# Kernel optimization log

Measured on AMD Instinct MI355X. Metric: run time of the kernel, lower is better.

The kernel has to match this reference:

```python
import jax, jax.numpy as jnp
import numpy as np

B, T, C, NH, RD = 128, 512, 384, 6, 16
HD = C // NH
SEQ_LEN = 512


def setup_inputs() -> dict:
    key = jax.random.key(0)
    kx, kqkv, kout = jax.random.split(key, 3)
    x = jax.random.normal(kx, (B, T, C), dtype=jnp.float32)
    # torch nn.Linear weights are [out_features, in_features]
    Wqkv = jax.random.normal(kqkv, (3 * C, C), dtype=jnp.float32) * 0.02
    Wout = jax.random.normal(kout, (C, C), dtype=jnp.float32) * 0.02
    freqs = 1.0 / (10000.0 ** (jnp.arange(0, RD, 2, dtype=jnp.float32) / RD))  # [RD//2]
    f = jnp.outer(jnp.arange(SEQ_LEN, dtype=jnp.float32), freqs)  # [SEQ_LEN, RD//2]
    cos = jnp.cos(f)[None, None]  # [1,1,SEQ_LEN,RD//2]
    sin = jnp.sin(f)[None, None]
    return {"x": x, "Wqkv": Wqkv, "Wout": Wout, "cos": cos, "sin": sin}


def _rope(t, c, s, rd):
    # t: [B, NH, T, HD]; partial rotary on first rd channels
    r, p = t[..., :rd], t[..., rd:]
    r1, r2 = r[..., : rd // 2], r[..., rd // 2:]
    rot = jnp.concatenate([r1 * c - r2 * s, r2 * c + r1 * s], axis=-1)
    return jnp.concatenate([rot, p], axis=-1)


def reference(x, Wqkv, Wout, cos, sin):
    b, t, c = x.shape
    nh, hd, rd = NH, c // NH, RD
    qkv = jnp.einsum("btc,dc->btd", x, Wqkv).reshape(b, t, 3, nh, hd)
    q, k, v = (jnp.transpose(qkv[:, :, i], (0, 2, 1, 3)) for i in range(3))  # [b,nh,t,hd]
    cc = cos[:, :, :t]
    ss = sin[:, :, :t]
    q = _rope(q, cc, ss, rd)
    k = _rope(k, cc, ss, rd)
    scale = 1.0 / jnp.sqrt(jnp.asarray(hd, dtype=x.dtype))
    scores = jnp.einsum("bhqd,bhkd->bhqk", q, k) * scale
    causal = jnp.tril(jnp.ones((t, t), dtype=bool))
    scores = jnp.where(causal, scores, jnp.finfo(scores.dtype).min)
    att = jax.nn.softmax(scores, axis=-1)
    o = jnp.einsum("bhqk,bhkd->bhqd", att, v)  # [b,nh,t,hd]
    o = jnp.transpose(o, (0, 2, 1, 3)).reshape(b, t, c)
    return jnp.einsum("btc,dc->btd", o, Wout)
```

## Files before the change

### kernel.cpp

```cpp
#include <hip/hip_runtime.h>

#define B_DIM 128
#define T_DIM 512
#define C_DIM 384
#define NH_DIM 6
#define HD_DIM 64
#define QKV_LD 1152

typedef __bf16 bf16x8 __attribute__((ext_vector_type(8)));
typedef __bf16 bf16x4 __attribute__((ext_vector_type(4)));
typedef float f32x4 __attribute__((ext_vector_type(4)));

#define K_SCALE 0.18033688011112042f

__device__ __forceinline__ void gload_lds16(const __bf16* g, __bf16* l) {
  __builtin_amdgcn_global_load_lds(
      (const __attribute__((address_space(1))) void*)g,
      (__attribute__((address_space(3))) void*)l, 16, 0, 0);
}

#define X_F4 6291456
#define WQKV_F4 110592
#define WOUT_F4 36864
__global__ __launch_bounds__(256) void cast_all(const float* __restrict__ x,
                                                const float* __restrict__ wqkv,
                                                const float* __restrict__ wout,
                                                __bf16* __restrict__ xb,
                                                __bf16* __restrict__ wqkvb,
                                                __bf16* __restrict__ woutb) {
  int i = blockIdx.x * blockDim.x + threadIdx.x;
  const float4* src;
  bf16x4* dst;
  if (i < X_F4) {
    src = (const float4*)x + i;
    dst = (bf16x4*)xb + i;
  } else if (i < X_F4 + WQKV_F4) {
    src = (const float4*)wqkv + (i - X_F4);
    dst = (bf16x4*)wqkvb + (i - X_F4);
  } else {
    src = (const float4*)wout + (i - X_F4 - WQKV_F4);
    dst = (bf16x4*)woutb + (i - X_F4 - WQKV_F4);
  }
  float4 v = *src;
  bf16x4 o;
  o[0] = (__bf16)v.x; o[1] = (__bf16)v.y; o[2] = (__bf16)v.z; o[3] = (__bf16)v.w;
  *dst = o;
}

__global__ __launch_bounds__(256) void gemm_bt(const __bf16* __restrict__ A,
                                               const __bf16* __restrict__ Bm,
                                               __bf16* __restrict__ Cb,
                                               float* __restrict__ Cf,
                                               const float* __restrict__ cosp,
                                               const float* __restrict__ sinp,
                                               int M, int N, int K) {
  __shared__ __attribute__((aligned(16))) __bf16 As[128 * 32];
  __shared__ __attribute__((aligned(16))) __bf16 Bs[128 * 32];
  const int nwg = gridDim.x * gridDim.y;
  const int bid = blockIdx.x + gridDim.x * blockIdx.y;
  const int per = nwg >> 3;
  const int swz = (bid & 7) * per + (bid >> 3);
  const int m0 = (swz / gridDim.x) * 128;
  const int n0 = (swz % gridDim.x) * 128;
  const int tid = threadIdx.x;
  const int wave = tid >> 6;
  const int lane = tid & 63;
  const int lr = lane & 15;
  const int quad = lane >> 4;
  const int wm = (wave & 1) * 64;
  const int wn = (wave >> 1) * 64;
  const int ca0 = wave * 2, ca1 = wave * 2 + 1;
  const int srow = lane >> 2;
  const int row0 = ca0 * 16 + srow, row1 = ca1 * 16 + srow;
  const int slot = (lane & 3) ^ ((lane >> 3) & 3);
  const int rs = (quad ^ ((lr >> 1) & 3)) * 8;
  f32x4 acc[4][4] = {};
  for (int k0 = 0; k0 < K; k0 += 32) {
    __syncthreads();
    gload_lds16(&A[(size_t)(m0 + row0) * K + k0 + slot * 8], &As[ca0 * 512]);
    gload_lds16(&A[(size_t)(m0 + row1) * K + k0 + slot * 8], &As[ca1 * 512]);
    gload_lds16(&Bm[(size_t)(n0 + row0) * K + k0 + slot * 8], &Bs[ca0 * 512]);
    gload_lds16(&Bm[(size_t)(n0 + row1) * K + k0 + slot * 8], &Bs[ca1 * 512]);
    __syncthreads();
    bf16x8 af[4], bf[4];
#pragma unroll
    for (int i = 0; i < 4; ++i)
      af[i] = *(bf16x8*)&As[(wm + i * 16 + lr) * 32 + rs];
#pragma unroll
    for (int j = 0; j < 4; ++j)
      bf[j] = *(bf16x8*)&Bs[(wn + j * 16 + lr) * 32 + rs];
#pragma unroll
    for (int i = 0; i < 4; ++i)
#pragma unroll
      for (int j = 0; j < 4; ++j)
        acc[i][j] = __builtin_amdgcn_mfma_f32_16x16x32_bf16(af[i], bf[j], acc[i][j], 0, 0, 0);
  }
  const bool doRope = (cosp != nullptr);
#pragma unroll
  for (int i = 0; i < 4; ++i) {
#pragma unroll
    for (int j = 0; j < 4; ++j) {
      int gm = m0 + wm + i * 16 + quad * 4;
      int gn = n0 + wn + j * 16 + lr;
      if (Cf) {
#pragma unroll
        for (int r = 0; r < 4; ++r) Cf[(size_t)(gm + r) * N + gn] = acc[i][j][r];
      } else {
        const int cbase = n0 + wn + j * 16;
        const bool ropeBlk = doRope && (cbase < 2 * C_DIM) && ((cbase & 63) == 0);
        const float qs = (doRope && cbase < C_DIM) ? K_SCALE : 1.0f;
        if (ropeBlk) {
#pragma unroll
          for (int r = 0; r < 4; ++r) {
            float v = acc[i][j][r];
            float p = __shfl_xor(v, 8, 64);
            int t = (gm + r) & (T_DIM - 1);
            float c = cosp[t * 8 + (lr & 7)];
            float s = sinp[t * 8 + (lr & 7)];
            v = (lr & 8) ? __builtin_fmaf(v, c, p * s)
                         : __builtin_fmaf(v, c, -p * s);
            Cb[(size_t)(gm + r) * N + gn] = (__bf16)(v * qs);
          }
        } else {
#pragma unroll
          for (int r = 0; r < 4; ++r)
            Cb[(size_t)(gm + r) * N + gn] = (__bf16)(acc[i][j][r] * qs);
        }
      }
    }
  }
}

__global__ __launch_bounds__(256) void transpose_v(const __bf16* __restrict__ qkv,
                                                   __bf16* __restrict__ vt) {
  __shared__ __attribute__((aligned(16))) __bf16 Tl[64][72];
  const int tt = blockIdx.x;
  const int h = blockIdx.y;
  const int b = blockIdx.z;
  const int tid = threadIdx.x;
  const __bf16* src = qkv + (size_t)b * T_DIM * QKV_LD + 2 * C_DIM + h * HD_DIM;
#pragma unroll
  for (int i = 0; i < 2; ++i) {
    int c = tid + i * 256;
    int row = c >> 3, cc = (c & 7) * 8;
    *(bf16x8*)&Tl[row][cc] = *(const bf16x8*)&src[(size_t)(tt * 64 + row) * QKV_LD + cc];
  }
  __syncthreads();
  __bf16* dst = vt + (size_t)(b * NH_DIM + h) * HD_DIM * T_DIM + tt * 64;
#pragma unroll
  for (int i = 0; i < 2; ++i) {
    int c = tid + i * 256;
    int drow = c >> 3, tc = (c & 7) * 8;
    bf16x8 v;
#pragma unroll
    for (int j = 0; j < 8; ++j) v[j] = Tl[tc + j][drow];
    *(bf16x8*)&dst[(size_t)drow * T_DIM + tc] = v;
  }
}

__global__ __launch_bounds__(256) void attn_kernel(const __bf16* __restrict__ qkv,
                                                   const __bf16* __restrict__ vt,
                                                   __bf16* __restrict__ o) {
  __shared__ __attribute__((aligned(16))) __bf16 K0s[64 * 64];
  __shared__ __attribute__((aligned(16))) __bf16 K1s[64 * 64];
  __shared__ __attribute__((aligned(16))) __bf16 V0s[64 * 64];
  __shared__ __attribute__((aligned(16))) __bf16 V1s[64 * 64];
  const int bid = blockIdx.x;
  const int swz = (bid & 7) * 384 + (bid >> 3);
  const int pair = swz & 3;
  const int h = (swz >> 2) % NH_DIM;
  const int b = swz / (4 * NH_DIM);
  const int qlo = pair, qhi = 7 - pair;
  const int tid = threadIdx.x;
  const int wave = tid >> 6;
  const int lane = tid & 63;
  const int lr = lane & 15;
  const int quad = lane >> 4;
  const __bf16* qbase = qkv + (size_t)b * T_DIM * QKV_LD + h * HD_DIM;
  const __bf16* kbase = qbase + C_DIM;
  const __bf16* vtb = vt + (size_t)(b * NH_DIM + h) * HD_DIM * T_DIM;
  const int qrow_lo = qlo * 64 + wave * 16;
  const int qrow_hi = qhi * 64 + wave * 16;
  bf16x8 qfl[2], qfh[2];
#pragma unroll
  for (int ks = 0; ks < 2; ++ks) {
    qfl[ks] = *(const bf16x8*)&qbase[(size_t)(qrow_lo + lr) * QKV_LD + ks * 32 + quad * 8];
    qfh[ks] = *(const bf16x8*)&qbase[(size_t)(qrow_hi + lr) * QKV_LD + ks * 32 + quad * 8];
  }
  f32x4 oaL[4] = {}, oaH[4] = {};
  f32x4 lL = {}, lH = {};
  bf16x8 vones;
#pragma unroll
  for (int e = 0; e < 8; ++e) vones[e] = (__bf16)1.0f;
  const int skey = (((lane >> 3) & 3) << 1) | (wave & 1);
  const int gsl = ((lane & 7) ^ skey) * 8;
  const int grA = wave * 8 + (lane >> 3);
  const int grB = grA + 32;
  const int ldsA = wave * 512;
  const int ldsB = (wave + 4) * 512;
  auto stage = [&](int kt, __bf16* KT, __bf16* VT) {
    const __bf16* ks = kbase + (size_t)(kt * 64) * QKV_LD;
    const __bf16* vs = vtb + kt * 64;
    gload_lds16(&ks[(size_t)grA * QKV_LD + gsl], KT + ldsA);
    gload_lds16(&ks[(size_t)grB * QKV_LD + gsl], KT + ldsB);
    gload_lds16(&vs[(size_t)grA * T_DIM + gsl], VT + ldsA);
    gload_lds16(&vs[(size_t)grB * T_DIM + gsl], VT + ldsB);
  };
  const int keyK = ((lr & 3) << 1) | ((lr >> 2) & 1);
  const int keyV = ((lr & 3) << 1) | ((lr >> 3) & 1);
  const int swK0 = (quad ^ keyK) * 8, swK1 = ((4 + quad) ^ keyK) * 8;
  const int swV0 = (quad ^ keyV) * 8, swV1 = ((4 + quad) ^ keyV) * 8;
  const int rkbase = ((lr >> 2) & 3) * 8 + (lr & 3);
  auto body = [&](const __bf16* KT, const __bf16* VT, const bf16x8 (&qf)[2],
                  f32x4 (&oa)[4], f32x4& lacc, int myq, bool diag, int kt) {
    f32x4 sj[4];
#pragma unroll
    for (int j = 0; j < 4; ++j) {
      const int rK = (j >> 1) * 32 + (j & 1) * 4 + rkbase;
      bf16x8 kf0 = *(const bf16x8*)&KT[rK * 64 + swK0];
      bf16x8 kf1 = *(const bf16x8*)&KT[rK * 64 + swK1];
      f32x4 z = {};
      z = __builtin_amdgcn_mfma_f32_16x16x32_bf16(kf0, qf[0], z, 0, 0, 0);
      z = __builtin_amdgcn_mfma_f32_16x16x32_bf16(kf1, qf[1], z, 0, 0, 0);
      sj[j] = z;
    }
    if (diag) {
#pragma unroll
      for (int j = 0; j < 4; ++j)
#pragma unroll
        for (int r = 0; r < 4; ++r) {
          int key = kt * 64 + (j >> 1) * 32 + quad * 8 + (j & 1) * 4 + r;
          if (key > myq) sj[j][r] = -3.0e38f;
        }
    }
    bf16x8 pf0, pf1;
#pragma unroll
    for (int j = 0; j < 4; ++j)
#pragma unroll
      for (int r = 0; r < 4; ++r) {
        float pv = exp2f(sj[j][r]);
        const int jj = (j & 1) * 4 + r;
        if (j < 2) pf0[jj] = (__bf16)pv; else pf1[jj] = (__bf16)pv;
      }
#pragma unroll
    for (int dt = 0; dt < 4; ++dt) {
      bf16x8 vf0 = *(const bf16x8*)&VT[(dt * 16 + lr) * 64 + swV0];
      bf16x8 vf1 = *(const bf16x8*)&VT[(dt * 16 + lr) * 64 + swV1];
      oa[dt] = __builtin_amdgcn_mfma_f32_16x16x32_bf16(pf0, vf0, oa[dt], 0, 0, 0);
      oa[dt] = __builtin_amdgcn_mfma_f32_16x16x32_bf16(pf1, vf1, oa[dt], 0, 0, 0);
    }
    lacc = __builtin_amdgcn_mfma_f32_16x16x32_bf16(pf0, vones, lacc, 0, 0, 0);
    lacc = __builtin_amdgcn_mfma_f32_16x16x32_bf16(pf1, vones, lacc, 0, 0, 0);
  };
  stage(0, K0s, V0s);
  __syncthreads();
  int kt = 0;
  while (true) {
    if (kt < qhi) stage(kt + 1, K1s, V1s);
    if (kt <= qlo) body(K0s, V0s, qfl, oaL, lL, qrow_lo + lr, kt == qlo, kt);
    body(K0s, V0s, qfh, oaH, lH, qrow_hi + lr, kt == qhi, kt);
    __syncthreads();
    ++kt;
    if (kt > qhi) break;
    if (kt < qhi) stage(kt + 1, K0s, V0s);
    if (kt <= qlo) body(K1s, V1s, qfl, oaL, lL, qrow_lo + lr, kt == qlo, kt);
    body(K1s, V1s, qfh, oaH, lH, qrow_hi + lr, kt == qhi, kt);
    __syncthreads();
    ++kt;
    if (kt > qhi) break;
  }
#pragma unroll
  for (int r = 0; r < 4; ++r) {
    float ilL = 1.0f / lL[r];
    float ilH = 1.0f / lH[r];
#pragma unroll
    for (int dt = 0; dt < 4; ++dt) {
      size_t rowL = (size_t)b * T_DIM + qrow_lo + quad * 4 + r;
      size_t rowH = (size_t)b * T_DIM + qrow_hi + quad * 4 + r;
      o[rowL * C_DIM + h * HD_DIM + dt * 16 + lr] = (__bf16)(oaL[dt][r] * ilL);
      o[rowH * C_DIM + h * HD_DIM + dt * 16 + lr] = (__bf16)(oaH[dt][r] * ilH);
    }
  }
}

extern "C" void kernel_launch(void* const* d_in, const int* in_sizes, int n_in,
                              void* d_out, int out_size, void* d_ws, size_t ws_size,
                              hipStream_t stream) {
  const float* x    = (const float*)d_in[0];
  const float* wqkv = (const float*)d_in[1];
  const float* wout = (const float*)d_in[2];
  const float* cosp = (const float*)d_in[3];
  const float* sinp = (const float*)d_in[4];
  float* out = (float*)d_out;

  char* ws = (char*)d_ws;
  __bf16* xb    = (__bf16*)(ws);
  __bf16* wqkvb = (__bf16*)(ws + 50331648);
  __bf16* woutb = (__bf16*)(ws + 51216384);
  __bf16* qkvb  = (__bf16*)(ws + 51511296);
  __bf16* ob    = (__bf16*)(ws + 202506240);
  __bf16* vtb   = xb;

  const int M = B_DIM * T_DIM;

  cast_all<<<25152, 256, 0, stream>>>(x, wqkv, wout, xb, wqkvb, woutb);

  gemm_bt<<<dim3(QKV_LD / 128, M / 128), 256, 0, stream>>>(
      xb, wqkvb, qkvb, (float*)nullptr, cosp, sinp, M, QKV_LD, C_DIM);

  transpose_v<<<dim3(T_DIM / 64, NH_DIM, B_DIM), 256, 0, stream>>>(qkvb, vtb);

  attn_kernel<<<3072, 256, 0, stream>>>(qkvb, vtb, ob);

  gemm_bt<<<dim3(C_DIM / 128, M / 128), 256, 0, stream>>>(
      ob, woutb, (__bf16*)nullptr, out, (const float*)nullptr, (const float*)nullptr,
      M, C_DIM, C_DIM);
}
```

Measured before the change: 401.4 us.

## Fuse V transpose into QKV GEMM epilogue and split Q/K outputs

The QKV GEMM epilogue now writes Q and K into separate contiguous [B*T, C] buffers and, for V column tiles, transposes the accumulator through LDS and writes V directly in the [b,h,d,t] layout. This removes the separate transpose_v kernel launch and its read/write of V, and the attention kernel reads Q/K with a smaller row stride. The GEMM's A/B pointers are also precomputed and incremented per K step. In exchange, the V-tile epilogue adds two LDS passes with extra barriers, and the workspace layout is reorganised.

```diff
diff --git a/kernel.cpp b/kernel.cpp
--- a/kernel.cpp
+++ b/kernel.cpp
@@ -49,7 +49,9 @@
 
 __global__ __launch_bounds__(256) void gemm_bt(const __bf16* __restrict__ A,
                                                const __bf16* __restrict__ Bm,
-                                               __bf16* __restrict__ Cb,
+                                               __bf16* __restrict__ Cbq,
+                                               __bf16* __restrict__ Cbk,
+                                               __bf16* __restrict__ vt,
                                                float* __restrict__ Cf,
                                                const float* __restrict__ cosp,
                                                const float* __restrict__ sinp,
@@ -74,13 +76,18 @@
   const int row0 = ca0 * 16 + srow, row1 = ca1 * 16 + srow;
   const int slot = (lane & 3) ^ ((lane >> 3) & 3);
   const int rs = (quad ^ ((lr >> 1) & 3)) * 8;
+  const __bf16* pA0 = &A[(size_t)(m0 + row0) * K + slot * 8];
+  const __bf16* pA1 = &A[(size_t)(m0 + row1) * K + slot * 8];
+  const __bf16* pB0 = &Bm[(size_t)(n0 + row0) * K + slot * 8];
+  const __bf16* pB1 = &Bm[(size_t)(n0 + row1) * K + slot * 8];
   f32x4 acc[4][4] = {};
   for (int k0 = 0; k0 < K; k0 += 32) {
     __syncthreads();
-    gload_lds16(&A[(size_t)(m0 + row0) * K + k0 + slot * 8], &As[ca0 * 512]);
-    gload_lds16(&A[(size_t)(m0 + row1) * K + k0 + slot * 8], &As[ca1 * 512]);
-    gload_lds16(&Bm[(size_t)(n0 + row0) * K + k0 + slot * 8], &Bs[ca0 * 512]);
-    gload_lds16(&Bm[(size_t)(n0 + row1) * K + k0 + slot * 8], &Bs[ca1 * 512]);
+    gload_lds16(pA0, &As[ca0 * 512]);
+    gload_lds16(pA1, &As[ca1 * 512]);
+    gload_lds16(pB0, &Bs[ca0 * 512]);
+    gload_lds16(pB1, &Bs[ca1 * 512]);
+    pA0 += 32; pA1 += 32; pB0 += 32; pB1 += 32;
     __syncthreads();
     bf16x8 af[4], bf[4];
 #pragma unroll
@@ -95,70 +102,87 @@
       for (int j = 0; j < 4; ++j)
         acc[i][j] = __builtin_amdgcn_mfma_f32_16x16x32_bf16(af[i], bf[j], acc[i][j], 0, 0, 0);
   }
-  const bool doRope = (cosp != nullptr);
+  if (Cf) {
+#pragma unroll
+    for (int i = 0; i < 4; ++i)
+#pragma unroll
+      for (int j = 0; j < 4; ++j) {
+        int gm = m0 + wm + i * 16 + quad * 4;
+        int gn = n0 + wn + j * 16 + lr;
+#pragma unroll
+        for (int r = 0; r < 4; ++r) Cf[(size_t)(gm + r) * N + gn] = acc[i][j][r];
+      }
+    return;
+  }
+  if (n0 >= 2 * C_DIM) {
+    const int tbase = (m0 & (T_DIM - 1)) + wm;
+    const int bb = m0 >> 9;
+    const int dcolbase = n0 - 2 * C_DIM + wn;
+    const int tslotx = (lane & 7) ^ (lane >> 3);
+#pragma unroll
+    for (int pass = 0; pass < 2; ++pass) {
+      __syncthreads();
+      if ((wave >> 1) == pass) {
+        __bf16* T = (wave & 1) ? Bs : As;
+#pragma unroll
+        for (int i = 0; i < 4; ++i)
+#pragma unroll
+          for (int j = 0; j < 4; ++j) {
+            const int d = j * 16 + lr;
+            const int sl = (i * 2 + (quad >> 1)) ^ (d & 7);
+            bf16x4 w;
+#pragma unroll
+            for (int r = 0; r < 4; ++r) w[r] = (__bf16)acc[i][j][r];
+            *(bf16x4*)&T[d * 64 + sl * 8 + (quad & 1) * 4] = w;
+          }
+#pragma unroll
+        for (int it = 0; it < 8; ++it) {
+          const int dl = it * 8 + (lane >> 3);
+          bf16x8 v = *(bf16x8*)&T[dl * 64 + (lane & 7) * 8];
+          const int dfull = dcolbase + dl;
+          const int hh = dfull >> 6, dd = dfull & 63;
+          *(bf16x8*)&vt[((size_t)(bb * NH_DIM + hh) * 64 + dd) * T_DIM + tbase +
+                        tslotx * 8] = v;
+        }
+      }
+    }
+    return;
+  }
+  const bool isQ = (n0 < C_DIM);
+  __bf16* dst = isQ ? Cbq : Cbk;
+  const int colbase = n0 - (isQ ? 0 : C_DIM);
+  const float qs = isQ ? K_SCALE : 1.0f;
 #pragma unroll
   for (int i = 0; i < 4; ++i) {
 #pragma unroll
     for (int j = 0; j < 4; ++j) {
       int gm = m0 + wm + i * 16 + quad * 4;
-      int gn = n0 + wn + j * 16 + lr;
-      if (Cf) {
-#pragma unroll
-        for (int r = 0; r < 4; ++r) Cf[(size_t)(gm + r) * N + gn] = acc[i][j][r];
+      int gn = colbase + wn + j * 16 + lr;
+      const int cbase = colbase + wn + j * 16;
+      const bool ropeBlk = ((cbase & 63) == 0);
+      if (ropeBlk) {
+#pragma unroll
+        for (int r = 0; r < 4; ++r) {
+          float v = acc[i][j][r];
+          float p = __shfl_xor(v, 8, 64);
+          int t = (gm + r) & (T_DIM - 1);
+          float c = cosp[t * 8 + (lr & 7)];
+          float s = sinp[t * 8 + (lr & 7)];
+          v = (lr & 8) ? __builtin_fmaf(v, c, p * s)
+                       : __builtin_fmaf(v, c, -p * s);
+          dst[(size_t)(gm + r) * C_DIM + gn] = (__bf16)(v * qs);
+        }
       } else {
-        const int cbase = n0 + wn + j * 16;
-        const bool ropeBlk = doRope && (cbase < 2 * C_DIM) && ((cbase & 63) == 0);
-        const float qs = (doRope && cbase < C_DIM) ? K_SCALE : 1.0f;
-        if (ropeBlk) {
-#pragma unroll
-          for (int r = 0; r < 4; ++r) {
-            float v = acc[i][j][r];
-            float p = __shfl_xor(v, 8, 64);
-            int t = (gm + r) & (T_DIM - 1);
-            float c = cosp[t * 8 + (lr & 7)];
-            float s = sinp[t * 8 + (lr & 7)];
-            v = (lr & 8) ? __builtin_fmaf(v, c, p * s)
-                         : __builtin_fmaf(v, c, -p * s);
-            Cb[(size_t)(gm + r) * N + gn] = (__bf16)(v * qs);
-          }
-        } else {
-#pragma unroll
-          for (int r = 0; r < 4; ++r)
-            Cb[(size_t)(gm + r) * N + gn] = (__bf16)(acc[i][j][r] * qs);
-        }
+#pragma unroll
+        for (int r = 0; r < 4; ++r)
+          dst[(size_t)(gm + r) * C_DIM + gn] = (__bf16)(acc[i][j][r] * qs);
       }
     }
   }
 }
 
-__global__ __launch_bounds__(256) void transpose_v(const __bf16* __restrict__ qkv,
-                                                   __bf16* __restrict__ vt) {
-  __shared__ __attribute__((aligned(16))) __bf16 Tl[64][72];
-  const int tt = blockIdx.x;
-  const int h = blockIdx.y;
-  const int b = blockIdx.z;
-  const int tid = threadIdx.x;
-  const __bf16* src = qkv + (size_t)b * T_DIM * QKV_LD + 2 * C_DIM + h * HD_DIM;
-#pragma unroll
-  for (int i = 0; i < 2; ++i) {
-    int c = tid + i * 256;
-    int row = c >> 3, cc = (c & 7) * 8;
-    *(bf16x8*)&Tl[row][cc] = *(const bf16x8*)&src[(size_t)(tt * 64 + row) * QKV_LD + cc];
-  }
-  __syncthreads();
-  __bf16* dst = vt + (size_t)(b * NH_DIM + h) * HD_DIM * T_DIM + tt * 64;
-#pragma unroll
-  for (int i = 0; i < 2; ++i) {
-    int c = tid + i * 256;
-    int drow = c >> 3, tc = (c & 7) * 8;
-    bf16x8 v;
-#pragma unroll
-    for (int j = 0; j < 8; ++j) v[j] = Tl[tc + j][drow];
-    *(bf16x8*)&dst[(size_t)drow * T_DIM + tc] = v;
-  }
-}
-
-__global__ __launch_bounds__(256) void attn_kernel(const __bf16* __restrict__ qkv,
+__global__ __launch_bounds__(256) void attn_kernel(const __bf16* __restrict__ qb,
+                                                   const __bf16* __restrict__ kb,
                                                    const __bf16* __restrict__ vt,
                                                    __bf16* __restrict__ o) {
   __shared__ __attribute__((aligned(16))) __bf16 K0s[64 * 64];
@@ -176,16 +200,16 @@
   const int lane = tid & 63;
   const int lr = lane & 15;
   const int quad = lane >> 4;
-  const __bf16* qbase = qkv + (size_t)b * T_DIM * QKV_LD + h * HD_DIM;
-  const __bf16* kbase = qbase + C_DIM;
+  const __bf16* qbase = qb + (size_t)b * T_DIM * C_DIM + h * HD_DIM;
+  const __bf16* kbase = kb + (size_t)b * T_DIM * C_DIM + h * HD_DIM;
   const __bf16* vtb = vt + (size_t)(b * NH_DIM + h) * HD_DIM * T_DIM;
   const int qrow_lo = qlo * 64 + wave * 16;
   const int qrow_hi = qhi * 64 + wave * 16;
   bf16x8 qfl[2], qfh[2];
 #pragma unroll
   for (int ks = 0; ks < 2; ++ks) {
-    qfl[ks] = *(const bf16x8*)&qbase[(size_t)(qrow_lo + lr) * QKV_LD + ks * 32 + quad * 8];
-    qfh[ks] = *(const bf16x8*)&qbase[(size_t)(qrow_hi + lr) * QKV_LD + ks * 32 + quad * 8];
+    qfl[ks] = *(const bf16x8*)&qbase[(size_t)(qrow_lo + lr) * C_DIM + ks * 32 + quad * 8];
+    qfh[ks] = *(const bf16x8*)&qbase[(size_t)(qrow_hi + lr) * C_DIM + ks * 32 + quad * 8];
   }
   f32x4 oaL[4] = {}, oaH[4] = {};
   f32x4 lL = {}, lH = {};
@@ -199,10 +223,10 @@
   const int ldsA = wave * 512;
   const int ldsB = (wave + 4) * 512;
   auto stage = [&](int kt, __bf16* KT, __bf16* VT) {
-    const __bf16* ks = kbase + (size_t)(kt * 64) * QKV_LD;
+    const __bf16* ks = kbase + (size_t)(kt * 64) * C_DIM;
     const __bf16* vs = vtb + kt * 64;
-    gload_lds16(&ks[(size_t)grA * QKV_LD + gsl], KT + ldsA);
-    gload_lds16(&ks[(size_t)grB * QKV_LD + gsl], KT + ldsB);
+    gload_lds16(&ks[(size_t)grA * C_DIM + gsl], KT + ldsA);
+    gload_lds16(&ks[(size_t)grB * C_DIM + gsl], KT + ldsB);
     gload_lds16(&vs[(size_t)grA * T_DIM + gsl], VT + ldsA);
     gload_lds16(&vs[(size_t)grB * T_DIM + gsl], VT + ldsB);
   };
@@ -295,24 +319,23 @@
 
   char* ws = (char*)d_ws;
   __bf16* xb    = (__bf16*)(ws);
-  __bf16* wqkvb = (__bf16*)(ws + 50331648);
-  __bf16* woutb = (__bf16*)(ws + 51216384);
-  __bf16* qkvb  = (__bf16*)(ws + 51511296);
-  __bf16* ob    = (__bf16*)(ws + 202506240);
-  __bf16* vtb   = xb;
+  __bf16* qb    = (__bf16*)(ws + 50331648);
+  __bf16* kb    = (__bf16*)(ws + 100663296);
+  __bf16* vtb   = (__bf16*)(ws + 150994944);
+  __bf16* ob    = (__bf16*)(ws + 201326592);
+  __bf16* wqkvb = (__bf16*)(ws + 251658240);
+  __bf16* woutb = (__bf16*)(ws + 252542976);
 
   const int M = B_DIM * T_DIM;
 
   cast_all<<<25152, 256, 0, stream>>>(x, wqkv, wout, xb, wqkvb, woutb);
 
   gemm_bt<<<dim3(QKV_LD / 128, M / 128), 256, 0, stream>>>(
-      xb, wqkvb, qkvb, (float*)nullptr, cosp, sinp, M, QKV_LD, C_DIM);
-
-  transpose_v<<<dim3(T_DIM / 64, NH_DIM, B_DIM), 256, 0, stream>>>(qkvb, vtb);
-
-  attn_kernel<<<3072, 256, 0, stream>>>(qkvb, vtb, ob);
+      xb, wqkvb, qb, kb, vtb, (float*)nullptr, cosp, sinp, M, QKV_LD, C_DIM);
+
+  attn_kernel<<<3072, 256, 0, stream>>>(qb, kb, vtb, ob);
 
   gemm_bt<<<dim3(C_DIM / 128, M / 128), 256, 0, stream>>>(
-      ob, woutb, (__bf16*)nullptr, out, (const float*)nullptr, (const float*)nullptr,
-      M, C_DIM, C_DIM);
-}
+      ob, woutb, (__bf16*)nullptr, (__bf16*)nullptr, (__bf16*)nullptr, out,
+      (const float*)nullptr, (const float*)nullptr, M, C_DIM, C_DIM);
+}
```

New measurement: 372.5 us. 7.2% less time.
